# Kernel optimization log

Measured on AMD Instinct MI355X. Metric: run time of the kernel, lower is better.

Reference implementation:

```python
import jax, jax.numpy as jnp
import numpy as np

B, H, W = 64, 128, 128
PS, G = 8, 16            # patch size, token grid (128//8)
E = 256                  # embed_dim (hidden_dim)
NS, IT, TEMP = 8, 3, 1.0 # num_slots, slot_iters, slot_temperature
V = 10                   # vocab_size
FD = 320                 # full_dim = latent_dim(256) + pose_dim(64)
HEADS, HD = 4, E // 4    # RoPE attn heads / head_dim
N = G * G


def _ln(x, g, b, eps=1e-5):
    m = x.mean(-1, keepdims=True)
    v = ((x - m) ** 2).mean(-1, keepdims=True)
    return (x - m) * jax.lax.rsqrt(v + eps) * g + b


def _conv(x, w, stride):
    return jax.lax.conv_general_dilated(
        x, w, (stride, stride), 'VALID',
        dimension_numbers=('NCHW', 'OIHW', 'NCHW'))


def _rope_tables(g, hd):
    half = hd // 2
    inv = 1.0 / (10000.0 ** (jnp.arange(0, half, 2, dtype=jnp.float32) / half))
    pos = jnp.arange(g, dtype=jnp.float32)
    p = jnp.outer(pos, inv)                                  # [g, half//2]
    e = jnp.concatenate([jnp.sin(p), jnp.cos(p)], axis=-1)   # [g, half]
    ex = jnp.broadcast_to(e[None, :, :], (g, g, half))
    ey = jnp.broadcast_to(e[:, None, :], (g, g, half))
    emb = jnp.concatenate([ey, ex], axis=-1).reshape(g * g, hd)
    return jnp.cos(emb)[None, :, None, :], jnp.sin(emb)[None, :, None, :]


def _apply_rope(x, cos, sin):
    x1, x2 = x[..., 0::2], x[..., 1::2]
    rot = jnp.concatenate([-x2, x1], axis=-1)
    return x * cos + rot * sin


def _gru(x, h, wih, whh, bih, bhh):
    gi = x @ wih.T + bih
    gh = h @ whh.T + bhh
    i_r, i_z, i_n = jnp.split(gi, 3, axis=-1)
    h_r, h_z, h_n = jnp.split(gh, 3, axis=-1)
    r = jax.nn.sigmoid(i_r + h_r)
    z = jax.nn.sigmoid(i_z + h_z)
    n = jnp.tanh(i_n + r * h_n)
    return (1.0 - z) * n + z * h


def setup_inputs() -> dict:
    key = jax.random.key(0)
    ks = iter(jax.random.split(key, 40))

    def nrm(shape, s=0.02):
        return (jax.random.normal(next(ks), shape, jnp.float32) * s)

    state = jax.random.randint(next(ks), (B, 1, H, W), 0, V).astype(jnp.float32)
    return {
        'state': state,
        'conv_w': nrm((E, 12, PS, PS)), 'conv_b': jnp.zeros((E,), jnp.float32),
        'mlp_ln_g': jnp.ones((E,), jnp.float32), 'mlp_ln_b': jnp.zeros((E,), jnp.float32),
        'mlp_w1': nrm((2 * E, E)), 'mlp_b1': jnp.zeros((2 * E,), jnp.float32),
        'mlp_w2': nrm((E, 2 * E)), 'mlp_b2': jnp.zeros((E,), jnp.float32),
        'qkv_w': nrm((3 * E, E)), 'qkv_b': jnp.zeros((3 * E,), jnp.float32),
        'proj_w': nrm((E, E)), 'proj_b': jnp.zeros((E,), jnp.float32),
        'ni_g': jnp.ones((E,), jnp.float32), 'ni_b': jnp.zeros((E,), jnp.float32),
        'ns_g': jnp.ones((FD,), jnp.float32), 'ns_b': jnp.zeros((FD,), jnp.float32),
        'nm_g': jnp.ones((FD,), jnp.float32), 'nm_b': jnp.zeros((FD,), jnp.float32),
        'q_w': nrm((FD, FD)), 'k_w': nrm((FD, E)), 'v_w': nrm((FD, E)),
        'gru_wih': nrm((3 * FD, FD)), 'gru_whh': nrm((3 * FD, FD)),
        'gru_bih': jnp.zeros((3 * FD,), jnp.float32), 'gru_bhh': jnp.zeros((3 * FD,), jnp.float32),
        'smlp_w1': nrm((2 * FD, FD)), 'smlp_b1': jnp.zeros((2 * FD,), jnp.float32),
        'smlp_w2': nrm((FD, 2 * FD)), 'smlp_b2': jnp.zeros((FD,), jnp.float32),
    }


def reference(state, conv_w, conv_b, mlp_ln_g, mlp_ln_b, mlp_w1, mlp_b1,
              mlp_w2, mlp_b2, qkv_w, qkv_b, proj_w, proj_b, ni_g, ni_b,
              ns_g, ns_b, nm_g, nm_b, q_w, k_w, v_w,
              gru_wih, gru_whh, gru_bih, gru_bhh,
              smlp_w1, smlp_b1, smlp_w2, smlp_b2):
    # Sobel edge features on replicate-padded image
    sob_x = jnp.array([[-1., 0., 1.], [-2., 0., 2.], [-1., 0., 1.]], jnp.float32).reshape(1, 1, 3, 3)
    sob_y = jnp.array([[-1., -2., -1.], [0., 0., 0.], [1., 2., 1.]], jnp.float32).reshape(1, 1, 3, 3)
    pad = jnp.pad(state, ((0, 0), (0, 0), (1, 1), (1, 1)), mode='edge')
    sx = _conv(pad, sob_x, 1)
    sy = _conv(pad, sob_y, 1)
    ids = jax.lax.stop_gradient(state)[:, 0].astype(jnp.int32)
    onehot = jax.nn.one_hot(ids, V, dtype=jnp.float32).transpose(0, 3, 1, 2)
    comp = jnp.concatenate([onehot, sx, sy], axis=1)            # [B,12,H,W]

    # Patch embed -> tokens [B,N,E]
    x = _conv(comp, conv_w, PS) + conv_b[None, :, None, None]   # [B,E,G,G]
    x = x.reshape(B, E, N).transpose(0, 2, 1)

    # patch_mlp (LN -> Linear -> GELU -> Linear), no residual
    h = _ln(x, mlp_ln_g, mlp_ln_b)
    h = jax.nn.gelu(h @ mlp_w1.T + mlp_b1, approximate=False)
    x = h @ mlp_w2.T + mlp_b2

    # RoPE self-attention, residual
    cos, sin = _rope_tables(G, HD)
    qkv = (x @ qkv_w.T + qkv_b).reshape(B, N, 3, HEADS, HD)
    q, k, v = qkv[:, :, 0], qkv[:, :, 1], qkv[:, :, 2]          # [B,N,Hh,HD]
    q = _apply_rope(q, cos, sin).transpose(0, 2, 1, 3)          # [B,Hh,N,HD]
    k = _apply_rope(k, cos, sin).transpose(0, 2, 1, 3)
    v = v.transpose(0, 2, 1, 3)
    attn = jax.nn.softmax(jnp.einsum('bhnd,bhmd->bhnm', q, k) * HD ** -0.5, axis=-1)
    ao = jnp.einsum('bhnm,bhmd->bhnd', attn, v).transpose(0, 2, 1, 3).reshape(B, N, E)
    x = x + (ao @ proj_w.T + proj_b)
    x = _ln(x, ni_g, ni_b)

    k_in = x @ k_w.T                                            # [B,N,FD]
    v_in = x @ v_w.T

    # No codebook injected -> zero slot priors
    slots = jnp.zeros((B, NS, FD), jnp.float32)
    sattn = None
    for _ in range(IT):
        slots_prev = slots
        q_s = _ln(slots, ns_g, ns_b) @ q_w.T                    # [B,NS,FD]
        logits = jnp.einsum('bnf,bsf->bns', k_in, q_s) * FD ** -0.5
        sattn = jax.nn.softmax(logits / TEMP, axis=-1)          # over slots
        an = sattn + 1e-8
        an = an / an.sum(axis=1, keepdims=True)                 # normalize over keys
        updates = jnp.einsum('bns,bnf->bsf', an, v_in)          # [B,NS,FD]
        slots = _gru(updates.reshape(-1, FD), slots_prev.reshape(-1, FD),
                     gru_wih, gru_whh, gru_bih, gru_bhh).reshape(B, NS, FD)
        m = _ln(slots, nm_g, nm_b)
        m = jax.nn.gelu(m @ smlp_w1.T + smlp_b1, approximate=False)
        slots = slots + (m @ smlp_w2.T + smlp_b2)

    masks = jax.lax.stop_gradient(sattn).transpose(0, 2, 1).reshape(B, NS, G, G)
    return slots, masks
```

## Files before the change

kernel.cpp:

```cpp
#include <hip/hip_runtime.h>
#include <math.h>

#define BB   64
#define HH   128
#define WW   128
#define GG   16
#define NN   256
#define EE   256
#define FD   320
#define NSL  8
#define NHEAD 4
#define HD   64
#define KIM  768

using short8 = __attribute__((ext_vector_type(8))) short;
using f32x4  = __attribute__((ext_vector_type(4))) float;

__device__ __forceinline__ float sigm(float x) { return 1.0f / (1.0f + expf(-x)); }
__device__ __forceinline__ float gelu_exact(float x) {
    return 0.5f * x * (1.0f + erff(x * 0.70710678118654752f));
}
__device__ __forceinline__ unsigned short f2b(float x) {
    unsigned u = __float_as_uint(x);
    u += 0x7fffu + ((u >> 16) & 1u);
    return (unsigned short)(u >> 16);
}
__device__ __forceinline__ float b2f(unsigned short u) {
    return __uint_as_float(((unsigned)u) << 16);
}
__device__ __forceinline__ void gload_lds16(const void* g, void* lds) {
    __builtin_amdgcn_global_load_lds(
        (const __attribute__((address_space(1))) unsigned int*)g,
        (__attribute__((address_space(3))) unsigned int*)lds, 16, 0, 0);
}
__device__ __forceinline__ void store_el(float* p, float v) { *p = v; }
__device__ __forceinline__ void store_el(unsigned short* p, float v) { *p = f2b(v); }

__global__ __launch_bounds__(256) void cvt_weights(
    const float* __restrict__ w0, const float* __restrict__ w1,
    const float* __restrict__ w2, const float* __restrict__ w3,
    const float* __restrict__ w4, const float* __restrict__ w5,
    const float* __restrict__ w6, const float* __restrict__ w7,
    const float* __restrict__ w8, const float* __restrict__ w9,
    const float* __restrict__ w10, const float* __restrict__ w11,
    unsigned short* __restrict__ dst) {
    int i = blockIdx.x * 256 + threadIdx.x;
    float v;
    if      (i <  196608) v = w0[i];
    else if (i <  327680) v = w1[i - 196608];
    else if (i <  458752) v = w2[i - 327680];
    else if (i <  655360) v = w3[i - 458752];
    else if (i <  720896) v = w4[i - 655360];
    else if (i <  802816) v = w5[i - 720896];
    else if (i <  884736) v = w6[i - 802816];
    else if (i <  987136) v = w7[i - 884736];
    else if (i < 1294336) v = w8[i - 987136];
    else if (i < 1601536) v = w9[i - 1294336];
    else if (i < 1806336) v = w10[i - 1601536];
    else                  v = w11[i - 1806336];
    dst[i] = f2b(v);
}

__global__ __launch_bounds__(256) void rope_tab(float* __restrict__ cs,
                                                float* __restrict__ sn) {
    int i = blockIdx.x * 256 + threadIdx.x;
    int d = i & 63, n = i >> 6;
    int pos = (d < 32) ? (n >> 4) : (n & 15);
    int j = d & 31;
    float freq = powf(10000.0f, -(float)(j & 15) / 16.0f);
    float p = (float)pos * freq;
    float ang = (j < 16) ? sinf(p) : cosf(p);
    cs[i] = cosf(ang);
    sn[i] = sinf(ang);
}

__global__ __launch_bounds__(256) void sobel_im2col(const float* __restrict__ state,
                                                    unsigned short* __restrict__ X0) {
    int idx = blockIdx.x * 256 + threadIdx.x;
    if (idx >= BB * HH * WW) return;
    int w = idx % WW;
    int h = (idx / WW) % HH;
    int b = idx / (HH * WW);
    const float* st = state + (long)b * HH * WW;
    auto at = [&](int y, int x) {
        y = min(max(y, 0), HH - 1);
        x = min(max(x, 0), WW - 1);
        return st[y * WW + x];
    };
    float v00 = at(h-1, w-1), v01 = at(h-1, w), v02 = at(h-1, w+1);
    float v10 = at(h,   w-1),                  v12 = at(h,   w+1);
    float v20 = at(h+1, w-1), v21 = at(h+1, w), v22 = at(h+1, w+1);
    float sx = (v02 - v00) + 2.0f * (v12 - v10) + (v22 - v20);
    float sy = (v20 - v00) + 2.0f * (v21 - v01) + (v22 - v02);
    int id = (int)st[h * WW + w];
    int gy = h >> 3, i = h & 7, gx = w >> 3, j = w & 7;
    long row = (long)b * NN + gy * GG + gx;
    unsigned short* xr = X0 + row * KIM + i * 8 + j;
#pragma unroll
    for (int c = 0; c < 10; c++) xr[c * 64] = (id == c) ? 0x3F80u : 0u;
    xr[10 * 64] = f2b(sx);
    xr[11 * 64] = f2b(sy);
}

template <int BM, int BN, int ACT>
__global__ __launch_bounds__(256) void gemm_bf16(
    const unsigned short* __restrict__ A, const unsigned short* __restrict__ W,
    const float* __restrict__ bias, const float* __restrict__ res,
    float* __restrict__ C, unsigned short* __restrict__ Cb,
    int K, long sA, long sW, long sC1, long sC2, int cdiv, int ldc, float scale)
{
    constexpr int WN = BN / 64;
    __shared__ __align__(16) unsigned short As[BM * 32];
    __shared__ __align__(16) unsigned short Bs[BN * 32];
    const int tid = threadIdx.x;
    const int w = tid >> 6, l = tid & 63;
    const int wm = w / WN, wn = w % WN;
    const int bz = blockIdx.z;
    const unsigned short* Ab = A + (long)bz * sA + (long)(blockIdx.y * BM) * K;
    const unsigned short* Wb = W + (long)bz * sW + (long)(blockIdx.x * BN) * K;
    const long offC = (long)(bz / cdiv) * sC1 + (long)(bz % cdiv) * sC2;

    const int rA  = l >> 2;
    const int swz = ((l & 3) ^ ((l >> 3) & 3)) * 8;

    f32x4 acc[4][4] = {};

    for (int k0 = 0; k0 < K; k0 += 32) {
#pragma unroll
        for (int c = 0; c < BM / 64; c++) {
            const int chunk = w * (BM / 64) + c;
            gload_lds16(Ab + (long)(chunk * 16 + rA) * K + k0 + swz, (char*)As + chunk * 1024);
        }
#pragma unroll
        for (int c = 0; c < BN / 64; c++) {
            const int chunk = w * (BN / 64) + c;
            gload_lds16(Wb + (long)(chunk * 16 + rA) * K + k0 + swz, (char*)Bs + chunk * 1024);
        }
        __syncthreads();
        short8 af[4], bfr[4];
#pragma unroll
        for (int m = 0; m < 4; m++) {
            const int row = wm * 64 + m * 16 + (l & 15);
            const int byte = row * 64 + (((l >> 4) ^ ((row >> 1) & 3)) << 4);
            af[m] = *(const short8*)((const char*)As + byte);
        }
#pragma unroll
        for (int n = 0; n < 4; n++) {
            const int row = wn * 64 + n * 16 + (l & 15);
            const int byte = row * 64 + (((l >> 4) ^ ((row >> 1) & 3)) << 4);
            bfr[n] = *(const short8*)((const char*)Bs + byte);
        }
#pragma unroll
        for (int m = 0; m < 4; m++)
#pragma unroll
            for (int n = 0; n < 4; n++)
                acc[m][n] = __builtin_amdgcn_mfma_f32_16x16x32_bf16(af[m], bfr[n], acc[m][n], 0, 0, 0);
        __syncthreads();
    }

    const int crow0 = blockIdx.y * BM + wm * 64;
    const int ccol0 = blockIdx.x * BN + wn * 64;
#pragma unroll
    for (int m = 0; m < 4; m++) {
#pragma unroll
        for (int n = 0; n < 4; n++) {
            const int row = crow0 + m * 16 + ((l >> 4) << 2);
            const int col = ccol0 + n * 16 + (l & 15);
#pragma unroll
            for (int r = 0; r < 4; r++) {
                float v = acc[m][n][r] * scale;
                if (bias) v += bias[col];
                if (ACT == 1) v = gelu_exact(v);
                const long idx = offC + (long)(row + r) * ldc + col;
                if (res) v += res[idx];
                if (C)  C[idx] = v;
                if (Cb) Cb[idx] = f2b(v);
            }
        }
    }
}

template <int ACT>
__global__ __launch_bounds__(256) void gemm_bf16_s(
    const unsigned short* __restrict__ A, const unsigned short* __restrict__ W,
    const float* __restrict__ bias0, const float* __restrict__ bias1,
    const float* __restrict__ res,
    float* __restrict__ C, unsigned short* __restrict__ Cb,
    int K, int N, long sA, long sW, long sC, float scale)
{
    __shared__ __align__(16) unsigned short As[64 * 32];
    __shared__ __align__(16) unsigned short Bs[64 * 32];
    const int tid = threadIdx.x;
    const int w = tid >> 6, l = tid & 63;
    const int gw = l >> 4, l15 = l & 15;
    const int bz = blockIdx.z;
    const unsigned short* Ab = A + (long)bz * sA + (long)(blockIdx.y * 64) * K;
    const unsigned short* Wb = W + (long)bz * sW + (long)(blockIdx.x * 64) * K;
    const float* bias = (bz == 0) ? bias0 : bias1;
    const long offC = (long)bz * sC;

    const int rA  = l >> 2;
    const int swz = ((l & 3) ^ ((l >> 3) & 3)) * 8;

    f32x4 acc[4] = {};

    for (int k0 = 0; k0 < K; k0 += 32) {
        gload_lds16(Ab + (long)(w * 16 + rA) * K + k0 + swz, (char*)As + w * 1024);
        gload_lds16(Wb + (long)(w * 16 + rA) * K + k0 + swz, (char*)Bs + w * 1024);
        __syncthreads();
        short8 af[4];
#pragma unroll
        for (int m = 0; m < 4; m++) {
            const int row = m * 16 + l15;
            af[m] = *(const short8*)((const char*)As + row * 64 + ((gw ^ ((row >> 1) & 3)) << 4));
        }
        const int brow = w * 16 + l15;
        const short8 bf = *(const short8*)((const char*)Bs + brow * 64 + ((gw ^ ((brow >> 1) & 3)) << 4));
#pragma unroll
        for (int m = 0; m < 4; m++)
            acc[m] = __builtin_amdgcn_mfma_f32_16x16x32_bf16(af[m], bf, acc[m], 0, 0, 0);
        __syncthreads();
    }

    const int col = blockIdx.x * 64 + w * 16 + l15;
    const int row0 = blockIdx.y * 64;
#pragma unroll
    for (int m = 0; m < 4; m++) {
        const int row = row0 + m * 16 + (gw << 2);
#pragma unroll
        for (int r = 0; r < 4; r++) {
            float v = acc[m][r] * scale;
            if (bias) v += bias[col];
            if (ACT == 1) v = gelu_exact(v);
            const long idx = offC + (long)(row + r) * N + col;
            if (res) v += res[idx];
            if (C)  C[idx] = v;
            if (Cb) Cb[idx] = f2b(v);
        }
    }
}

template <typename OT>
__global__ __launch_bounds__(256) void ln_rows(const float* __restrict__ X,
                                               OT* __restrict__ Y,
                                               const float* __restrict__ g,
                                               const float* __restrict__ b,
                                               int rows, int D) {
    int gtid = blockIdx.x * 256 + threadIdx.x;
    int row = gtid >> 6;
    int lane = gtid & 63;
    if (row >= rows) return;
    const float* x = X + (long)row * D;
    const int nv = D >> 6;
    float v[5];
    float s = 0.0f;
#pragma unroll 5
    for (int i = 0; i < nv; i++) { v[i] = x[lane + (i << 6)]; s += v[i]; }
#pragma unroll
    for (int o = 32; o; o >>= 1) s += __shfl_down(s, o);
    s = __shfl(s, 0);
    float mean = s / (float)D;
    float s2 = 0.0f;
#pragma unroll 5
    for (int i = 0; i < nv; i++) { float d = v[i] - mean; s2 += d * d; }
#pragma unroll
    for (int o = 32; o; o >>= 1) s2 += __shfl_down(s2, o);
    s2 = __shfl(s2, 0);
    float inv = rsqrtf(s2 / (float)D + 1e-5f);
    OT* y = Y + (long)row * D;
#pragma unroll 5
    for (int i = 0; i < nv; i++) {
        int d = lane + (i << 6);
        store_el(&y[d], (v[i] - mean) * inv * g[d] + b[d]);
    }
}

__global__ __launch_bounds__(256) void gru_ln(const float* __restrict__ GI,
                                              const float* __restrict__ GH,
                                              float* __restrict__ slots,
                                              const float* __restrict__ g,
                                              const float* __restrict__ b,
                                              unsigned short* __restrict__ SLnb) {
    int gtid = blockIdx.x * 256 + threadIdx.x;
    int row = gtid >> 6;
    int lane = gtid & 63;
    const float* gi = GI + (long)row * 960;
    const float* gh = GH + (long)row * 960;
    float* sl = slots + (long)row * FD;
    float h[5];
    float s = 0.0f;
#pragma unroll
    for (int i = 0; i < 5; i++) {
        const int f = lane + (i << 6);
        const float rr = sigm(gi[f] + gh[f]);
        const float z  = sigm(gi[320 + f] + gh[320 + f]);
        const float nn = tanhf(gi[640 + f] + rr * gh[640 + f]);
        const float hn = (1.0f - z) * nn + z * sl[f];
        h[i] = hn;
        s += hn;
        sl[f] = hn;
    }
#pragma unroll
    for (int o = 32; o; o >>= 1) s += __shfl_down(s, o);
    s = __shfl(s, 0);
    const float mean = s * (1.0f / FD);
    float s2 = 0.0f;
#pragma unroll
    for (int i = 0; i < 5; i++) { const float d = h[i] - mean; s2 += d * d; }
#pragma unroll
    for (int o = 32; o; o >>= 1) s2 += __shfl_down(s2, o);
    s2 = __shfl(s2, 0);
    const float inv = rsqrtf(s2 * (1.0f / FD) + 1e-5f);
    unsigned short* y = SLnb + (long)row * FD;
#pragma unroll
    for (int i = 0; i < 5; i++) {
        const int f = lane + (i << 6);
        y[f] = f2b((h[i] - mean) * inv * g[f] + b[f]);
    }
}

__global__ __launch_bounds__(256) void rope_qk(const unsigned short* __restrict__ QKVb,
                                               const float* __restrict__ cs,
                                               const float* __restrict__ sn,
                                               unsigned short* __restrict__ Qr,
                                               unsigned short* __restrict__ Kr) {
    const int rid = blockIdx.x * 256 + threadIdx.x;
    const int n = rid & 255;
    const int h = (rid >> 8) & 3;
    const int b = rid >> 10;
    const unsigned short* src = QKVb + ((long)(b * 256 + n)) * 768 + h * 64;
    float cv[64], sv[64];
#pragma unroll
    for (int i = 0; i < 16; i++) {
        *(float4*)&cv[i * 4] = *(const float4*)(cs + n * 64 + i * 4);
        *(float4*)&sv[i * 4] = *(const float4*)(sn + n * 64 + i * 4);
    }
#pragma unroll
    for (int qk = 0; qk < 2; qk++) {
        const unsigned short* s0 = src + qk * 256;
        unsigned short* dst = (qk == 0 ? Qr : Kr) + (long)rid * 64;
        float x[64];
#pragma unroll
        for (int i = 0; i < 8; i++) {
            short8 v = *(const short8*)(s0 + i * 8);
#pragma unroll
            for (int j = 0; j < 8; j++) x[i * 8 + j] = b2f((unsigned short)v[j]);
        }
        unsigned short o[64];
#pragma unroll
        for (int d = 0; d < 64; d++) {
            const float rot = (d < 32) ? -x[2 * d + 1] : x[2 * (d - 32)];
            o[d] = f2b(x[d] * cv[d] + rot * sv[d]);
        }
#pragma unroll
        for (int i = 0; i < 8; i++)
            *(short8*)(dst + i * 8) = *(short8*)&o[i * 8];
    }
}

__global__ __launch_bounds__(256, 1) void fused_attn(
    const unsigned short* __restrict__ Qr,
    const unsigned short* __restrict__ Kr,
    const unsigned short* __restrict__ QKVb,
    unsigned short* __restrict__ AOb)
{
    __shared__ __align__(16) char SL[49152];
    const int h = blockIdx.x, b = blockIdx.y;
    const int tid = threadIdx.x;
    const int w = tid >> 6, l = tid & 63;
    const int gw = l >> 4, l15 = l & 15;
    const long bh = (long)b * 4 + h;
    const unsigned short* Qb = Qr + bh * NN * 64;
    const unsigned short* Kb = Kr + bh * NN * 64;

    {
        const int n0 = (tid & 127) * 2;
        const int dh = tid >> 7;
        const unsigned short* v0p = QKVb + ((long)b * NN + n0) * 768 + h * 64 + 512 + dh * 32;
        const unsigned short* v1p = v0p + 768;
        unsigned short v0[32], v1[32];
#pragma unroll
        for (int i = 0; i < 4; i++) {
            *(short8*)&v0[i * 8] = *(const short8*)(v0p + i * 8);
            *(short8*)&v1[i * 8] = *(const short8*)(v1p + i * 8);
        }
#pragma unroll
        for (int i = 0; i < 32; i++) {
            const int d = dh * 32 + i;
            const unsigned val = (unsigned)v0[i] | ((unsigned)v1[i] << 16);
            *(unsigned*)(SL + d * 512 + (((n0 >> 3) ^ (d & 15)) << 4) + (n0 & 7) * 2) = val;
        }
    }
    __syncthreads();

    char* Pw = SL + 32768 + w * 4096;

#pragma unroll
    for (int p = 0; p < 2; p++) {
        const int mbase = w * 64 + p * 32;
        f32x4 accs[16][2] = {};
#pragma unroll
        for (int kk = 0; kk < 2; kk++) {
            short8 bq[2];
#pragma unroll
            for (int mf = 0; mf < 2; mf++)
                bq[mf] = *(const short8*)(Qb + ((mbase + mf * 16 + l15) << 6) + kk * 32 + gw * 8);
#pragma unroll
            for (int nf = 0; nf < 16; nf++) {
                const short8 ak = *(const short8*)(Kb + ((nf * 16 + l15) << 6) + kk * 32 + gw * 8);
#pragma unroll
                for (int mf = 0; mf < 2; mf++)
                    accs[nf][mf] = __builtin_amdgcn_mfma_f32_16x16x32_bf16(ak, bq[mf], accs[nf][mf], 0, 0, 0);
            }
        }
        float rs[2];
#pragma unroll
        for (int mf = 0; mf < 2; mf++) {
            float mx = -1e30f;
#pragma unroll
            for (int nf = 0; nf < 16; nf++)
#pragma unroll
                for (int r = 0; r < 4; r++) mx = fmaxf(mx, accs[nf][mf][r]);
            mx = fmaxf(mx, __shfl_xor(mx, 16));
            mx = fmaxf(mx, __shfl_xor(mx, 32));
            float sum = 0.0f;
#pragma unroll
            for (int nf = 0; nf < 16; nf++)
#pragma unroll
                for (int r = 0; r < 4; r++) {
                    const float e = expf((accs[nf][mf][r] - mx) * 0.125f);
                    accs[nf][mf][r] = e;
                    sum += e;
                }
            sum += __shfl_xor(sum, 16);
            sum += __shfl_xor(sum, 32);
            rs[mf] = 1.0f / sum;
        }
        f32x4 acco[4][2] = {};
#pragma unroll
        for (int c = 0; c < 4; c++) {
#pragma unroll
            for (int nfi = 0; nfi < 4; nfi++) {
                const int nf = c * 4 + nfi;
                const int kt = nf >> 1;
                const int gr = (nf & 1) * 2 + (gw >> 1);
                const int lr = l15 + 16 * gr;
                const int j0 = (gw & 1) * 4;
#pragma unroll
                for (int mf = 0; mf < 2; mf++) {
                    uint2 pk;
                    pk.x = (unsigned)f2b(accs[nf][mf][0] * rs[mf]) |
                           ((unsigned)f2b(accs[nf][mf][1] * rs[mf]) << 16);
                    pk.y = (unsigned)f2b(accs[nf][mf][2] * rs[mf]) |
                           ((unsigned)f2b(accs[nf][mf][3] * rs[mf]) << 16);
                    *(uint2*)(Pw + ((kt & 1) * 2 + mf) * 1024 + lr * 16 + j0 * 2) = pk;
                }
            }
#pragma unroll
            for (int kti = 0; kti < 2; kti++) {
                const int kt = c * 2 + kti;
                short8 vf[4];
#pragma unroll
                for (int df = 0; df < 4; df++) {
                    const int d = df * 16 + l15;
                    vf[df] = *(const short8*)(SL + d * 512 + (((kt * 4 + gw) ^ (d & 15)) << 4));
                }
#pragma unroll
                for (int mf = 0; mf < 2; mf++) {
                    const short8 pf = *(const short8*)(Pw + (kti * 2 + mf) * 1024 + l * 16);
#pragma unroll
                    for (int df = 0; df < 4; df++)
                        acco[df][mf] = __builtin_amdgcn_mfma_f32_16x16x32_bf16(vf[df], pf, acco[df][mf], 0, 0, 0);
                }
            }
        }
#pragma unroll
        for (int df = 0; df < 4; df++)
#pragma unroll
            for (int mf = 0; mf < 2; mf++) {
                const int m = mbase + mf * 16 + l15;
                const int d = df * 16 + gw * 4;
                unsigned short o[4];
#pragma unroll
                for (int r = 0; r < 4; r++) o[r] = f2b(acco[df][mf][r]);
                *(uint2*)(AOb + ((long)(b * NN + m) * 256 + h * 64 + d)) = *(uint2*)o;
            }
    }
}

__global__ __launch_bounds__(256) void slot_logits(const float* __restrict__ Kin,
                                                   const float* __restrict__ Qs,
                                                   float* __restrict__ sattn,
                                                   float* __restrict__ sums2,
                                                   float* __restrict__ mout) {
    const int b = blockIdx.x;
    const int chunk = blockIdx.y;
    __shared__ float qs[NSL][FD];
    __shared__ float colsum[NSL];
    const int tid = threadIdx.x;
    for (int i = tid; i < NSL * FD; i += 256) qs[i / FD][i % FD] = Qs[(long)b * NSL * FD + i];
    if (tid < NSL) colsum[tid] = 0.0f;
    __syncthreads();
    const int wv = tid >> 6, lane = tid & 63;
    float wsum[NSL] = {};
#pragma unroll
    for (int rr = 0; rr < 4; rr++) {
        const int r = chunk * 16 + wv * 4 + rr;
        const float* kr = Kin + ((long)b * NN + r) * FD;
        float acc[NSL] = {};
#pragma unroll
        for (int i = 0; i < 5; i++) {
            const int t = lane + (i << 6);
            const float kv = kr[t];
#pragma unroll
            for (int s = 0; s < NSL; s++) acc[s] = fmaf(kv, qs[s][t], acc[s]);
        }
#pragma unroll
        for (int s = 0; s < NSL; s++)
#pragma unroll
            for (int o = 32; o; o >>= 1) acc[s] += __shfl_down(acc[s], o);
        if (lane == 0) {
            const float scale = 0.055901699437494740f;
            float mx = -1e30f;
#pragma unroll
            for (int s = 0; s < NSL; s++) { acc[s] *= scale; mx = fmaxf(mx, acc[s]); }
            float e[NSL], sum = 0.0f;
#pragma unroll
            for (int s = 0; s < NSL; s++) { e[s] = expf(acc[s] - mx); sum += e[s]; }
            const float rsum = 1.0f / sum;
            float* outp = sattn + ((long)b * NN + r) * NSL;
#pragma unroll
            for (int s = 0; s < NSL; s++) {
                const float pp = e[s] * rsum;
                outp[s] = pp;
                wsum[s] += pp;
                if (mout) mout[(long)b * 2048 + s * 256 + r] = pp;
            }
        }
    }
    if (lane == 0) {
#pragma unroll
        for (int s = 0; s < NSL; s++) atomicAdd(&colsum[s], wsum[s]);
    }
    __syncthreads();
    if (tid < NSL) sums2[((long)(b << 4) + chunk) * NSL + tid] = colsum[tid];
}

__global__ __launch_bounds__(256) void slot_updates(const float* __restrict__ sattn,
                                                    const float* __restrict__ sums2,
                                                    const float* __restrict__ Vin,
                                                    unsigned short* __restrict__ Updb) {
    const int b = blockIdx.x;
    const int tid = threadIdx.x;
    const int w = tid >> 6, l = tid & 63;
    __shared__ float inv_s[NSL];
    __shared__ float an_s[NN][NSL];
    __shared__ float red[4][NSL][FD];
    if (tid < NSL) {
        float tot = (float)NN * 1e-8f;
#pragma unroll
        for (int c = 0; c < 16; c++) tot += sums2[((long)(b << 4) + c) * NSL + tid];
        inv_s[tid] = 1.0f / tot;
    }
    __syncthreads();
    {
        const float4 p0 = *(const float4*)(sattn + ((long)b * NN + tid) * NSL);
        const float4 p1 = *(const float4*)(sattn + ((long)b * NN + tid) * NSL + 4);
        an_s[tid][0] = (p0.x + 1e-8f) * inv_s[0];
        an_s[tid][1] = (p0.y + 1e-8f) * inv_s[1];
        an_s[tid][2] = (p0.z + 1e-8f) * inv_s[2];
        an_s[tid][3] = (p0.w + 1e-8f) * inv_s[3];
        an_s[tid][4] = (p1.x + 1e-8f) * inv_s[4];
        an_s[tid][5] = (p1.y + 1e-8f) * inv_s[5];
        an_s[tid][6] = (p1.z + 1e-8f) * inv_s[6];
        an_s[tid][7] = (p1.w + 1e-8f) * inv_s[7];
    }
    __syncthreads();
    float acc[NSL][5] = {};
    const float* vb = Vin + ((long)b * NN + w * 64) * FD;
    for (int i = 0; i < 64; i++) {
        float v[5];
#pragma unroll
        for (int j = 0; j < 5; j++) v[j] = vb[(long)i * FD + l + (j << 6)];
        float a[NSL];
#pragma unroll
        for (int s = 0; s < NSL; s++) a[s] = an_s[w * 64 + i][s];
#pragma unroll
        for (int s = 0; s < NSL; s++)
#pragma unroll
            for (int j = 0; j < 5; j++)
                acc[s][j] = fmaf(a[s], v[j], acc[s][j]);
    }
#pragma unroll
    for (int s = 0; s < NSL; s++)
#pragma unroll
        for (int j = 0; j < 5; j++)
            red[w][s][l + (j << 6)] = acc[s][j];
    __syncthreads();
    for (int idx = tid; idx < NSL * FD; idx += 256) {
        const int s = idx / FD, f = idx % FD;
        const float tot = red[0][s][f] + red[1][s][f] + red[2][s][f] + red[3][s][f];
        Updb[((long)b * NSL + s) * FD + f] = f2b(tot);
    }
}

extern "C" void kernel_launch(void* const* d_in, const int* in_sizes, int n_in,
                              void* d_out, int out_size, void* d_ws, size_t ws_size,
                              hipStream_t stream) {
    const float* state    = (const float*)d_in[0];
    const float* conv_w   = (const float*)d_in[1];
    const float* conv_b   = (const float*)d_in[2];
    const float* mlp_ln_g = (const float*)d_in[3];
    const float* mlp_ln_b = (const float*)d_in[4];
    const float* mlp_w1   = (const float*)d_in[5];
    const float* mlp_b1   = (const float*)d_in[6];
    const float* mlp_w2   = (const float*)d_in[7];
    const float* mlp_b2   = (const float*)d_in[8];
    const float* qkv_w    = (const float*)d_in[9];
    const float* qkv_b    = (const float*)d_in[10];
    const float* proj_w   = (const float*)d_in[11];
    const float* proj_b   = (const float*)d_in[12];
    const float* ni_g     = (const float*)d_in[13];
    const float* ni_b     = (const float*)d_in[14];
    const float* ns_g     = (const float*)d_in[15];
    const float* ns_b     = (const float*)d_in[16];
    const float* nm_g     = (const float*)d_in[17];
    const float* nm_b     = (const float*)d_in[18];
    const float* q_w      = (const float*)d_in[19];
    const float* k_w      = (const float*)d_in[20];
    const float* v_w      = (const float*)d_in[21];
    const float* gru_wih  = (const float*)d_in[22];
    const float* gru_whh  = (const float*)d_in[23];
    const float* gru_bih  = (const float*)d_in[24];
    const float* gru_bhh  = (const float*)d_in[25];
    const float* smlp_w1  = (const float*)d_in[26];
    const float* smlp_b1  = (const float*)d_in[27];
    const float* smlp_w2  = (const float*)d_in[28];
    const float* smlp_b2  = (const float*)d_in[29];

    float* ws = (float*)d_ws;
    const int M = BB * NN;
    typedef unsigned short u16;

    u16*   X0b  = (u16*)(ws + 0L);
    u16*   Qr   = (u16*)(ws + 0L);
    u16*   Kr   = (u16*)(ws + 2097152L);
    float* X1   = ws + 6291456L;
    u16*   XLNb = (u16*)(ws + 10485760L);
    u16*   Hbufb= (u16*)(ws + 12582912L);
    u16*   QKVb = (u16*)(ws + 6291456L);
    u16*   X2b  = (u16*)(ws + 23068672L);
    float* X2   = ws + 31457280L;
    u16*   Xnb  = (u16*)(ws + 31457280L);
    float* X3   = ws + 35651584L;
    float* Slots= ws + 35651584L;
    float* Qs   = ws + 35979264L;
    float* Satt = ws + 36143104L;
    float* Sums2= ws + 36274176L;
    float* GI   = ws + 36438528L;
    float* GH   = ws + 36930048L;
    u16*   SLnb = (u16*)(ws + 37421568L);
    u16*   Updb = (u16*)(ws + 37503488L);
    u16*   Slotsb=(u16*)(ws + 37585408L);
    u16*   Mhb  = (u16*)(ws + 37667328L);
    float* Kin  = ws + 39845888L;
    float* Vin  = ws + 45088768L;
    u16*   AOb    = (u16*)(ws + 50331648L);
    u16*   wb     = (u16*)(ws + 52428800L);
    u16*   conv_wb= wb + 0;
    u16*   mlp_w1b= wb + 196608;
    u16*   mlp_w2b= wb + 327680;
    u16*   qkv_wb = wb + 458752;
    u16*   proj_wb= wb + 655360;
    u16*   k_wb   = wb + 720896;
    u16*   v_wb   = wb + 802816;
    u16*   q_wb   = wb + 884736;
    u16*   wihb   = wb + 987136;
    u16*   whhb   = wb + 1294336;
    u16*   smlp1b = wb + 1601536;
    u16*   smlp2b = wb + 1806336;
    float* CS     = ws + 53434368L;
    float* SN     = ws + 53450752L;

    float* out = (float*)d_out;

    auto gemmA = [&](const u16* A, const u16* Wt, const float* bias, const float* res,
                     float* C, u16* Cb, int Mm, int Nn, int Kk, int batch,
                     long sA, long sW, long sC1, long sC2, int cdiv, int ldc,
                     float scale, int act) {
        dim3 grid(Nn / 128, Mm / 128, batch);
        if (act) gemm_bf16<128, 128, 1><<<grid, 256, 0, stream>>>(A, Wt, bias, res, C, Cb, Kk, sA, sW, sC1, sC2, cdiv, ldc, scale);
        else     gemm_bf16<128, 128, 0><<<grid, 256, 0, stream>>>(A, Wt, bias, res, C, Cb, Kk, sA, sW, sC1, sC2, cdiv, ldc, scale);
    };
    auto gemmB = [&](const u16* A, const u16* Wt, float* C, int Mm, int Nn, int Kk) {
        dim3 grid(Nn / 64, Mm / 256, 1);
        gemm_bf16<256, 64, 0><<<grid, 256, 0, stream>>>(A, Wt, nullptr, nullptr, C, nullptr, Kk, 0, 0, 0, 0, 1, Nn, 1.0f);
    };
    auto gemmS = [&](const u16* A, const u16* Wt, const float* b0, const float* b1,
                     const float* res, float* C, u16* Cb, int Mm, int Nn, int Kk,
                     int batch, long sA, long sW, long sC, int act) {
        dim3 grid(Nn / 64, Mm / 64, batch);
        if (act) gemm_bf16_s<1><<<grid, 256, 0, stream>>>(A, Wt, b0, b1, res, C, Cb, Kk, Nn, sA, sW, sC, 1.0f);
        else     gemm_bf16_s<0><<<grid, 256, 0, stream>>>(A, Wt, b0, b1, res, C, Cb, Kk, Nn, sA, sW, sC, 1.0f);
    };

    cvt_weights<<<dim3(2011136 / 256), 256, 0, stream>>>(conv_w, mlp_w1, mlp_w2, qkv_w,
                                                         proj_w, k_w, v_w, q_w,
                                                         gru_wih, gru_whh, smlp_w1, smlp_w2, wb);
    rope_tab<<<dim3(16384 / 256), 256, 0, stream>>>(CS, SN);

    sobel_im2col<<<dim3((BB * HH * WW) / 256), 256, 0, stream>>>(state, X0b);
    gemmA(X0b, conv_wb, conv_b, nullptr, X1, nullptr, M, EE, KIM, 1, 0, 0, 0, 0, 1, EE, 1.0f, 0);
    ln_rows<u16><<<dim3(M * 64 / 256), 256, 0, stream>>>(X1, XLNb, mlp_ln_g, mlp_ln_b, M, EE);
    gemmA(XLNb, mlp_w1b, mlp_b1, nullptr, nullptr, Hbufb, M, 2 * EE, EE, 1, 0, 0, 0, 0, 1, 2 * EE, 1.0f, 1);
    gemmA(Hbufb, mlp_w2b, mlp_b2, nullptr, X2, X2b, M, EE, 2 * EE, 1, 0, 0, 0, 0, 1, EE, 1.0f, 0);
    gemmA(X2b, qkv_wb, qkv_b, nullptr, nullptr, QKVb, M, 3 * EE, EE, 1, 0, 0, 0, 0, 1, 3 * EE, 1.0f, 0);
    rope_qk<<<dim3(65536 / 256), 256, 0, stream>>>(QKVb, CS, SN, Qr, Kr);
    fused_attn<<<dim3(NHEAD, BB), 256, 0, stream>>>(Qr, Kr, QKVb, AOb);
    gemmA(AOb, proj_wb, proj_b, X2, X3, nullptr, M, EE, EE, 1, 0, 0, 0, 0, 1, EE, 1.0f, 0);
    ln_rows<u16><<<dim3(M * 64 / 256), 256, 0, stream>>>(X3, Xnb, ni_g, ni_b, M, EE);
    gemmB(Xnb, k_wb, Kin, M, FD, EE);
    gemmB(Xnb, v_wb, Vin, M, FD, EE);
    hipMemsetAsync(Slots, 0, (size_t)BB * NSL * FD * sizeof(float), stream);
    hipMemsetAsync(Slotsb, 0, (size_t)BB * NSL * FD * sizeof(u16), stream);
    for (int it = 0; it < 3; it++) {
        ln_rows<u16><<<dim3(512 * 64 / 256), 256, 0, stream>>>(Slots, SLnb, ns_g, ns_b, 512, FD);
        gemmS(SLnb, q_wb, nullptr, nullptr, nullptr, Qs, nullptr, 512, FD, FD, 1, 0, 0, 0, 0);
        slot_logits<<<dim3(BB, 16), 256, 0, stream>>>(Kin, Qs, Satt, Sums2,
                                                      (it == 2) ? (out + 163840) : nullptr);
        slot_updates<<<dim3(BB), 256, 0, stream>>>(Satt, Sums2, Vin, Updb);
        gemmS(Updb, wihb, gru_bih, gru_bhh, nullptr, GI, nullptr, 512, 960, FD,
              2, 163840, 307200, 491520, 0);
        gru_ln<<<dim3(512 * 64 / 256), 256, 0, stream>>>(GI, GH, Slots, nm_g, nm_b, SLnb);
        gemmS(SLnb, smlp1b, smlp_b1, nullptr, nullptr, nullptr, Mhb, 512, 2 * FD, FD, 1, 0, 0, 0, 1);
        if (it < 2)
            gemmS(Mhb, smlp2b, smlp_b2, nullptr, Slots, Slots, Slotsb, 512, FD, 2 * FD, 1, 0, 0, 0, 0);
        else
            gemmS(Mhb, smlp2b, smlp_b2, nullptr, Slots, out, nullptr, 512, FD, 2 * FD, 1, 0, 0, 0, 0);
    }
}
```

Before: 627.0 us.

## Merge K/V projections into one bf16 GEMM and split attention blocks over query halves

Fuses the two slot-attention K and V projection GEMMs into a single GEMM with a 640-wide output stored as interleaved bf16 rows. The slot_logits and slot_updates kernels now read the bf16 K and V halves, which cuts global memory traffic in the three slot iterations and removes one launch. Separately, fused_attn's two-pass query loop becomes a third grid dimension, doubling block count for more parallelism at the cost of staging V into LDS twice. Keeping K and V in bf16 instead of fp32 lowers precision of the slot logits and updates.

Measured after the change: 618.1 us. Within noise of the previous version (-1.4%).

```diff
diff --git a/kernel.cpp b/kernel.cpp
--- a/kernel.cpp
+++ b/kernel.cpp
@@ -366,6 +366,7 @@
 {
     __shared__ __align__(16) char SL[49152];
     const int h = blockIdx.x, b = blockIdx.y;
+    const int p = blockIdx.z;
     const int tid = threadIdx.x;
     const int w = tid >> 6, l = tid & 63;
     const int gw = l >> 4, l15 = l & 15;
@@ -395,8 +396,7 @@
 
     char* Pw = SL + 32768 + w * 4096;
 
-#pragma unroll
-    for (int p = 0; p < 2; p++) {
+    {
         const int mbase = w * 64 + p * 32;
         f32x4 accs[16][2] = {};
 #pragma unroll
@@ -488,7 +488,7 @@
     }
 }
 
-__global__ __launch_bounds__(256) void slot_logits(const float* __restrict__ Kin,
+__global__ __launch_bounds__(256) void slot_logits(const unsigned short* __restrict__ KVin,
                                                    const float* __restrict__ Qs,
                                                    float* __restrict__ sattn,
                                                    float* __restrict__ sums2,
@@ -506,12 +506,12 @@
 #pragma unroll
     for (int rr = 0; rr < 4; rr++) {
         const int r = chunk * 16 + wv * 4 + rr;
-        const float* kr = Kin + ((long)b * NN + r) * FD;
+        const unsigned short* kr = KVin + ((long)b * NN + r) * 640;
         float acc[NSL] = {};
 #pragma unroll
         for (int i = 0; i < 5; i++) {
             const int t = lane + (i << 6);
-            const float kv = kr[t];
+            const float kv = b2f(kr[t]);
 #pragma unroll
             for (int s = 0; s < NSL; s++) acc[s] = fmaf(kv, qs[s][t], acc[s]);
         }
@@ -548,7 +548,7 @@
 
 __global__ __launch_bounds__(256) void slot_updates(const float* __restrict__ sattn,
                                                     const float* __restrict__ sums2,
-                                                    const float* __restrict__ Vin,
+                                                    const unsigned short* __restrict__ KVin,
                                                     unsigned short* __restrict__ Updb) {
     const int b = blockIdx.x;
     const int tid = threadIdx.x;
@@ -577,11 +577,11 @@
     }
     __syncthreads();
     float acc[NSL][5] = {};
-    const float* vb = Vin + ((long)b * NN + w * 64) * FD;
+    const unsigned short* vb = KVin + ((long)b * NN + w * 64) * 640 + 320;
     for (int i = 0; i < 64; i++) {
         float v[5];
 #pragma unroll
-        for (int j = 0; j < 5; j++) v[j] = vb[(long)i * FD + l + (j << 6)];
+        for (int j = 0; j < 5; j++) v[j] = b2f(vb[(long)i * 640 + l + (j << 6)]);
         float a[NSL];
 #pragma unroll
         for (int s = 0; s < NSL; s++) a[s] = an_s[w * 64 + i][s];
@@ -663,8 +663,7 @@
     u16*   Updb = (u16*)(ws + 37503488L);
     u16*   Slotsb=(u16*)(ws + 37585408L);
     u16*   Mhb  = (u16*)(ws + 37667328L);
-    float* Kin  = ws + 39845888L;
-    float* Vin  = ws + 45088768L;
+    u16*   KVinb= (u16*)(ws + 39845888L);
     u16*   AOb    = (u16*)(ws + 50331648L);
     u16*   wb     = (u16*)(ws + 52428800L);
     u16*   conv_wb= wb + 0;
@@ -672,8 +671,7 @@
     u16*   mlp_w2b= wb + 327680;
     u16*   qkv_wb = wb + 458752;
     u16*   proj_wb= wb + 655360;
-    u16*   k_wb   = wb + 720896;
-    u16*   v_wb   = wb + 802816;
+    u16*   kv_wb  = wb + 720896;
     u16*   q_wb   = wb + 884736;
     u16*   wihb   = wb + 987136;
     u16*   whhb   = wb + 1294336;
@@ -692,9 +690,9 @@
         if (act) gemm_bf16<128, 128, 1><<<grid, 256, 0, stream>>>(A, Wt, bias, res, C, Cb, Kk, sA, sW, sC1, sC2, cdiv, ldc, scale);
         else     gemm_bf16<128, 128, 0><<<grid, 256, 0, stream>>>(A, Wt, bias, res, C, Cb, Kk, sA, sW, sC1, sC2, cdiv, ldc, scale);
     };
-    auto gemmB = [&](const u16* A, const u16* Wt, float* C, int Mm, int Nn, int Kk) {
+    auto gemmB = [&](const u16* A, const u16* Wt, u16* Cb, int Mm, int Nn, int Kk) {
         dim3 grid(Nn / 64, Mm / 256, 1);
-        gemm_bf16<256, 64, 0><<<grid, 256, 0, stream>>>(A, Wt, nullptr, nullptr, C, nullptr, Kk, 0, 0, 0, 0, 1, Nn, 1.0f);
+        gemm_bf16<256, 64, 0><<<grid, 256, 0, stream>>>(A, Wt, nullptr, nullptr, nullptr, Cb, Kk, 0, 0, 0, 0, 1, Nn, 1.0f);
     };
     auto gemmS = [&](const u16* A, const u16* Wt, const float* b0, const float* b1,
                      const float* res, float* C, u16* Cb, int Mm, int Nn, int Kk,
@@ -716,19 +714,18 @@
     gemmA(Hbufb, mlp_w2b, mlp_b2, nullptr, X2, X2b, M, EE, 2 * EE, 1, 0, 0, 0, 0, 1, EE, 1.0f, 0);
     gemmA(X2b, qkv_wb, qkv_b, nullptr, nullptr, QKVb, M, 3 * EE, EE, 1, 0, 0, 0, 0, 1, 3 * EE, 1.0f, 0);
     rope_qk<<<dim3(65536 / 256), 256, 0, stream>>>(QKVb, CS, SN, Qr, Kr);
-    fused_attn<<<dim3(NHEAD, BB), 256, 0, stream>>>(Qr, Kr, QKVb, AOb);
+    fused_attn<<<dim3(NHEAD, BB, 2), 256, 0, stream>>>(Qr, Kr, QKVb, AOb);
     gemmA(AOb, proj_wb, proj_b, X2, X3, nullptr, M, EE, EE, 1, 0, 0, 0, 0, 1, EE, 1.0f, 0);
     ln_rows<u16><<<dim3(M * 64 / 256), 256, 0, stream>>>(X3, Xnb, ni_g, ni_b, M, EE);
-    gemmB(Xnb, k_wb, Kin, M, FD, EE);
-    gemmB(Xnb, v_wb, Vin, M, FD, EE);
+    gemmB(Xnb, kv_wb, KVinb, M, 640, EE);
     hipMemsetAsync(Slots, 0, (size_t)BB * NSL * FD * sizeof(float), stream);
     hipMemsetAsync(Slotsb, 0, (size_t)BB * NSL * FD * sizeof(u16), stream);
     for (int it = 0; it < 3; it++) {
         ln_rows<u16><<<dim3(512 * 64 / 256), 256, 0, stream>>>(Slots, SLnb, ns_g, ns_b, 512, FD);
         gemmS(SLnb, q_wb, nullptr, nullptr, nullptr, Qs, nullptr, 512, FD, FD, 1, 0, 0, 0, 0);
-        slot_logits<<<dim3(BB, 16), 256, 0, stream>>>(Kin, Qs, Satt, Sums2,
+        slot_logits<<<dim3(BB, 16), 256, 0, stream>>>(KVinb, Qs, Satt, Sums2,
                                                       (it == 2) ? (out + 163840) : nullptr);
-        slot_updates<<<dim3(BB), 256, 0, stream>>>(Satt, Sums2, Vin, Updb);
+        slot_updates<<<dim3(BB), 256, 0, stream>>>(Satt, Sums2, KVinb, Updb);
         gemmS(Updb, wihb, gru_bih, gru_bhh, nullptr, GI, nullptr, 512, 960, FD,
               2, 163840, 307200, 491520, 0);
         gru_ln<<<dim3(512 * 64 / 256), 256, 0, stream>>>(GI, GH, Slots, nm_g, nm_b, SLnb);
```
